# Performance work log

Hardware: AMD Instinct MI355X
Metric: run time of the kernel (lower is better)

## Reference

```python
import jax, jax.numpy as jnp
import numpy as np

GAMMA = 1.0  # weight on CRL loss
BETA = 1.0   # weight on MDCA calibration loss
B, C = 4096, 32000
DATASET_SIZE = 50000


def setup_inputs() -> dict:
    key = jax.random.key(0)
    k1, k2, k3, k4 = jax.random.split(key, 4)
    logits = jax.random.normal(k1, (B, C), dtype=jnp.float32)
    targets = jax.random.randint(k2, (B,), 0, C, dtype=jnp.int64)
    idx = jax.random.randint(k3, (B,), 0, DATASET_SIZE, dtype=jnp.int64)
    # normalized historical correctness per dataset sample (History table)
    correctness = jax.random.uniform(k4, (DATASET_SIZE,), dtype=jnp.float32)
    return {"logits": logits, "targets": targets, "idx": idx, "correctness": correctness}


def reference(logits, targets, idx, correctness):
    b, c = logits.shape
    logp = jax.nn.log_softmax(logits, axis=1)
    # CrossEntropyLoss (mean reduction)
    loss_cls = -jnp.mean(jnp.take_along_axis(logp, targets[:, None], axis=1))
    p = jnp.exp(logp)  # softmax probabilities, reused by MDCA and CRL

    # MDCA: mean_c | mean_b p[:, c] - freq(target == c) |, fused (no per-class loop)
    avg_conf = jnp.mean(p, axis=0)                                  # [C]
    avg_count = jnp.zeros((c,), logits.dtype).at[targets].add(1.0) / b  # [C]
    loss_cal = jnp.mean(jnp.abs(avg_conf - avg_count))

    # CRL (rank_target='softmax'): max-softmax confidence margin ranking
    conf = jnp.max(p, axis=1)          # [B]
    conf2 = jnp.roll(conf, -1)
    idx2 = jnp.roll(idx, -1)
    c1 = correctness[idx]
    c2 = correctness[idx2]
    rank_target = jnp.sign(c1 - c2)                     # {-1, 0, +1}
    rank_margin = jnp.abs(c1 - c2)
    tnz = jnp.where(rank_target == 0, jnp.ones_like(rank_target), rank_target)
    rank_input2 = conf2 + rank_margin / tnz
    # MarginRankingLoss(margin=0, mean): mean(max(0, -target*(x1 - x2)))
    loss_ref = jnp.mean(jnp.maximum(0.0, -rank_target * (conf - rank_input2)))

    return loss_cls + GAMMA * loss_ref + BETA * loss_cal
```

## Files before the change

### kernel.cpp

```cpp
#include <hip/hip_runtime.h>
#include <math.h>


#define NB  256
#define TPB 1024
#define NJ  8

__global__ __launch_bounds__(TPB) void fused_pass_kernel(
    const float* __restrict__ logits, const int* __restrict__ targets,
    float* __restrict__ partial,
    float* __restrict__ rowinv, float* __restrict__ celogp,
    float* __restrict__ counts, int B, int C)
{
    const int tid = threadIdx.x;
    const int n4  = C >> 2;
    const int rpb = B / NB;
    const int r0  = blockIdx.x * rpb;

    __shared__ float red[2][TPB / 64];
    __shared__ float sS[64];

    float4 acc[NJ];
    #pragma unroll
    for (int j = 0; j < NJ; ++j) acc[j] = make_float4(0.f, 0.f, 0.f, 0.f);

    const int wid = tid >> 6;

    float4 f[NJ], g[NJ];

    {
        const float4* row4 = (const float4*)(logits + (size_t)r0 * (size_t)C);
        #pragma unroll
        for (int j = 0; j < NJ; ++j) {
            const int k = tid + TPB * j;
            f[j] = (k < n4) ? row4[k] : make_float4(-1e30f, -1e30f, -1e30f, -1e30f);
        }
    }

    for (int r = 0; r < rpb; ++r) {
        if (r + 1 < rpb) {
            const float4* nrow =
                (const float4*)(logits + (size_t)(r0 + r + 1) * (size_t)C);
            #pragma unroll
            for (int j = 0; j < NJ; ++j) {
                const int k = tid + TPB * j;
                g[j] = (k < n4) ? nrow[k]
                                : make_float4(-1e30f, -1e30f, -1e30f, -1e30f);
            }
        }

        float ls = 0.f;
        #pragma unroll
        for (int j = 0; j < NJ; ++j) {
            f[j].x = __expf(f[j].x);
            f[j].y = __expf(f[j].y);
            f[j].z = __expf(f[j].z);
            f[j].w = __expf(f[j].w);
            ls += (f[j].x + f[j].y) + (f[j].z + f[j].w);
        }

        #pragma unroll
        for (int off = 32; off; off >>= 1) ls += __shfl_xor(ls, off, 64);
        const int par = r & 1;
        if ((tid & 63) == 0) red[par][wid] = ls;
        __syncthreads();
        float s = 0.f;
        #pragma unroll
        for (int w = 0; w < TPB / 64; ++w) s += red[par][w];
        if (tid == 0) sS[r] = s;
        const float inv = 1.0f / s;

        #pragma unroll
        for (int j = 0; j < NJ; ++j) {
            acc[j].x = fmaf(f[j].x, inv, acc[j].x);
            acc[j].y = fmaf(f[j].y, inv, acc[j].y);
            acc[j].z = fmaf(f[j].z, inv, acc[j].z);
            acc[j].w = fmaf(f[j].w, inv, acc[j].w);
        }

        if (r + 1 < rpb) {
            #pragma unroll
            for (int j = 0; j < NJ; ++j) f[j] = g[j];
        }
    }

    float4* po = (float4*)(partial + (size_t)blockIdx.x * (size_t)C);
    #pragma unroll
    for (int j = 0; j < NJ; ++j) {
        const int k = tid + TPB * j;
        if (k < n4) po[k] = acc[j];
    }

    __syncthreads();
    if (tid < rpb) {
        const int b = r0 + tid;
        const float s = sS[tid];
        rowinv[b] = 1.0f / s;
        const int t = targets[b];
        celogp[b] = logits[(size_t)b * (size_t)C + t] - logf(s);
        atomicAdd(&counts[t], 1.0f);
    }
}

__global__ __launch_bounds__(256) void reduce_cal_kernel(
    const float* __restrict__ partial, const float* __restrict__ counts,
    float* __restrict__ cal, int C)
{
    const int n4  = C >> 2;
    const int tid = threadIdx.x;
    const int c4  = blockIdx.x * 32 + (tid & 31);
    const int pg  = tid >> 5;

    const float4* p4   = (const float4*)partial;
    const float4* base = p4 + (size_t)(pg * (NB / 8)) * (size_t)n4 + c4;

    float4 s = make_float4(0.f, 0.f, 0.f, 0.f);
    #pragma unroll
    for (int p = 0; p < NB / 8; ++p) {
        const float4 v = base[(size_t)p * (size_t)n4];
        s.x += v.x; s.y += v.y; s.z += v.z; s.w += v.w;
    }

    __shared__ float4 lds[8][32];
    lds[pg][tid & 31] = s;
    __syncthreads();

    if (tid < 32) {
        float4 t = lds[0][tid];
        #pragma unroll
        for (int gi = 1; gi < 8; ++gi) {
            const float4 v = lds[gi][tid];
            t.x += v.x; t.y += v.y; t.z += v.z; t.w += v.w;
        }
        const float4 cnt = ((const float4*)counts)[c4];
        float d = fabsf(t.x - cnt.x) + fabsf(t.y - cnt.y)
                + fabsf(t.z - cnt.z) + fabsf(t.w - cnt.w);
        #pragma unroll
        for (int off = 16; off; off >>= 1) d += __shfl_xor(d, off, 64);
        if (tid == 0) atomicAdd(cal, d);
    }
}

__global__ __launch_bounds__(1024) void final_loss_kernel(
    const float* __restrict__ rowinv, const float* __restrict__ celogp,
    const int* __restrict__ idx, const float* __restrict__ correctness,
    const float* __restrict__ cal, float* __restrict__ out, int B, int C)
{
    const int tid = threadIdx.x;
    float sum_ce = 0.f, sum_crl = 0.f;

    for (int b = tid; b < B; b += 1024) {
        sum_ce += celogp[b];
        const int b2 = (b + 1 == B) ? 0 : b + 1;
        const float conf  = rowinv[b];
        const float conf2 = rowinv[b2];
        const float c1 = correctness[idx[b]];
        const float c2 = correctness[idx[b2]];
        const float rt  = (c1 > c2) ? 1.f : ((c1 < c2) ? -1.f : 0.f);
        const float rm  = fabsf(c1 - c2);
        const float tnz = (rt == 0.f) ? 1.f : rt;
        const float ri2 = conf2 + rm / tnz;
        sum_crl += fmaxf(0.f, -rt * (conf - ri2));
    }

    #pragma unroll
    for (int off = 32; off; off >>= 1) {
        sum_ce  += __shfl_xor(sum_ce,  off, 64);
        sum_crl += __shfl_xor(sum_crl, off, 64);
    }
    __shared__ float red[2][16];
    const int wid = tid >> 6;
    if ((tid & 63) == 0) { red[0][wid] = sum_ce; red[1][wid] = sum_crl; }
    __syncthreads();
    if (tid == 0) {
        float tce = 0.f, tcrl = 0.f;
        #pragma unroll
        for (int w = 0; w < 16; ++w) { tce += red[0][w]; tcrl += red[1][w]; }
        const float loss_cls = -tce / (float)B;
        const float loss_ref = tcrl / (float)B;
        const float loss_cal = cal[0] / ((float)B * (float)C);
        out[0] = loss_cls + loss_ref + loss_cal;
    }
}

extern "C" void kernel_launch(void* const* d_in, const int* in_sizes, int n_in,
                              void* d_out, int out_size, void* d_ws, size_t ws_size,
                              hipStream_t stream) {
    const float* logits      = (const float*)d_in[0];
    const int*   targets     = (const int*)d_in[1];
    const int*   idx         = (const int*)d_in[2];
    const float* correctness = (const float*)d_in[3];
    float* out = (float*)d_out;

    const int B = in_sizes[1];
    const int C = in_sizes[0] / B;

    char* ws = (char*)d_ws;
    float* partial = (float*)ws;   ws += (size_t)NB * (size_t)C * sizeof(float);
    float* rowinv  = (float*)ws;   ws += (size_t)B * sizeof(float);
    float* celogp  = (float*)ws;   ws += (size_t)B * sizeof(float);
    float* counts  = (float*)ws;   ws += (size_t)C * sizeof(float);
    float* cal     = (float*)ws;

    hipMemsetAsync(counts, 0, (size_t)C * sizeof(float), stream);
    hipMemsetAsync(cal, 0, sizeof(float), stream);

    fused_pass_kernel<<<NB, TPB, 0, stream>>>(logits, targets, partial,
                                              rowinv, celogp, counts, B, C);

    reduce_cal_kernel<<<(C >> 2) / 32, 256, 0, stream>>>(partial, counts, cal, C);

    final_loss_kernel<<<1, 1024, 0, stream>>>(rowinv, celogp, idx, correctness,
                                              cal, out, B, C);
}
```

Before: 791.2 us.

## Split fused pass into separate row-sum and column-sum kernels

Replaces the single fused kernel, which computed row sums and column accumulations with a block-wide barrier per row, with two kernels. The first kernel uses one block per row to compute the softmax denominator, CE term and target counts. The second re-reads the logits and accumulates the normalized exp per column using the precomputed inverse sums. This removes the per-row __syncthreads and register double-buffering and gives the row pass more parallelism, at the cost of reading the 524 MB logits matrix twice and computing exp twice.

```diff
diff --git a/kernel.cpp b/kernel.cpp
--- a/kernel.cpp
+++ b/kernel.cpp
@@ -6,81 +6,73 @@
 #define TPB 1024
 #define NJ  8
 
-__global__ __launch_bounds__(TPB) void fused_pass_kernel(
+__global__ __launch_bounds__(256) void rowsum_kernel(
     const float* __restrict__ logits, const int* __restrict__ targets,
-    float* __restrict__ partial,
     float* __restrict__ rowinv, float* __restrict__ celogp,
-    float* __restrict__ counts, int B, int C)
+    float* __restrict__ counts, int C)
+{
+    const int b   = blockIdx.x;
+    const int tid = threadIdx.x;
+    const int n4  = C >> 2;
+    const int nfull = n4 >> 8;
+    const int rem   = n4 - (nfull << 8);
+
+    const float4* row4 = (const float4*)(logits + (size_t)b * (size_t)C);
+
+    float ls = 0.f;
+    #pragma unroll 4
+    for (int i = 0; i < nfull; ++i) {
+        const float4 v = row4[tid + (i << 8)];
+        ls += (__expf(v.x) + __expf(v.y)) + (__expf(v.z) + __expf(v.w));
+    }
+    if (tid < rem) {
+        const float4 v = row4[(nfull << 8) + tid];
+        ls += (__expf(v.x) + __expf(v.y)) + (__expf(v.z) + __expf(v.w));
+    }
+
+    #pragma unroll
+    for (int off = 32; off; off >>= 1) ls += __shfl_xor(ls, off, 64);
+    __shared__ float red[4];
+    if ((tid & 63) == 0) red[tid >> 6] = ls;
+    __syncthreads();
+    if (tid == 0) {
+        const float s = red[0] + red[1] + red[2] + red[3];
+        rowinv[b] = 1.0f / s;
+        const int t = targets[b];
+        celogp[b] = logits[(size_t)b * (size_t)C + t] - logf(s);
+        atomicAdd(&counts[t], 1.0f);
+    }
+}
+
+__global__ __launch_bounds__(TPB) void colsum_kernel(
+    const float* __restrict__ logits, const float* __restrict__ rowinv,
+    float* __restrict__ partial, int B, int C)
 {
     const int tid = threadIdx.x;
     const int n4  = C >> 2;
     const int rpb = B / NB;
     const int r0  = blockIdx.x * rpb;
 
-    __shared__ float red[2][TPB / 64];
-    __shared__ float sS[64];
-
     float4 acc[NJ];
     #pragma unroll
     for (int j = 0; j < NJ; ++j) acc[j] = make_float4(0.f, 0.f, 0.f, 0.f);
 
-    const int wid = tid >> 6;
+    for (int r = 0; r < rpb; ++r) {
+        const float4* row4 = (const float4*)(logits + (size_t)(r0 + r) * (size_t)C);
+        const float inv = rowinv[r0 + r];
 
-    float4 f[NJ], g[NJ];
-
-    {
-        const float4* row4 = (const float4*)(logits + (size_t)r0 * (size_t)C);
+        float4 f[NJ];
         #pragma unroll
         for (int j = 0; j < NJ; ++j) {
             const int k = tid + TPB * j;
             f[j] = (k < n4) ? row4[k] : make_float4(-1e30f, -1e30f, -1e30f, -1e30f);
         }
-    }
-
-    for (int r = 0; r < rpb; ++r) {
-        if (r + 1 < rpb) {
-            const float4* nrow =
-                (const float4*)(logits + (size_t)(r0 + r + 1) * (size_t)C);
-            #pragma unroll
-            for (int j = 0; j < NJ; ++j) {
-                const int k = tid + TPB * j;
-                g[j] = (k < n4) ? nrow[k]
-                                : make_float4(-1e30f, -1e30f, -1e30f, -1e30f);
-            }
-        }
-
-        float ls = 0.f;
         #pragma unroll
         for (int j = 0; j < NJ; ++j) {
-            f[j].x = __expf(f[j].x);
-            f[j].y = __expf(f[j].y);
-            f[j].z = __expf(f[j].z);
-            f[j].w = __expf(f[j].w);
-            ls += (f[j].x + f[j].y) + (f[j].z + f[j].w);
-        }
-
-        #pragma unroll
-        for (int off = 32; off; off >>= 1) ls += __shfl_xor(ls, off, 64);
-        const int par = r & 1;
-        if ((tid & 63) == 0) red[par][wid] = ls;
-        __syncthreads();
-        float s = 0.f;
-        #pragma unroll
-        for (int w = 0; w < TPB / 64; ++w) s += red[par][w];
-        if (tid == 0) sS[r] = s;
-        const float inv = 1.0f / s;
-
-        #pragma unroll
-        for (int j = 0; j < NJ; ++j) {
-            acc[j].x = fmaf(f[j].x, inv, acc[j].x);
-            acc[j].y = fmaf(f[j].y, inv, acc[j].y);
-            acc[j].z = fmaf(f[j].z, inv, acc[j].z);
-            acc[j].w = fmaf(f[j].w, inv, acc[j].w);
-        }
-
-        if (r + 1 < rpb) {
-            #pragma unroll
-            for (int j = 0; j < NJ; ++j) f[j] = g[j];
+            acc[j].x = fmaf(__expf(f[j].x), inv, acc[j].x);
+            acc[j].y = fmaf(__expf(f[j].y), inv, acc[j].y);
+            acc[j].z = fmaf(__expf(f[j].z), inv, acc[j].z);
+            acc[j].w = fmaf(__expf(f[j].w), inv, acc[j].w);
         }
     }
 
@@ -89,16 +81,6 @@
     for (int j = 0; j < NJ; ++j) {
         const int k = tid + TPB * j;
         if (k < n4) po[k] = acc[j];
-    }
-
-    __syncthreads();
-    if (tid < rpb) {
-        const int b = r0 + tid;
-        const float s = sS[tid];
-        rowinv[b] = 1.0f / s;
-        const int t = targets[b];
-        celogp[b] = logits[(size_t)b * (size_t)C + t] - logf(s);
-        atomicAdd(&counts[t], 1.0f);
     }
 }
 
@@ -205,8 +187,10 @@
     hipMemsetAsync(counts, 0, (size_t)C * sizeof(float), stream);
     hipMemsetAsync(cal, 0, sizeof(float), stream);
 
-    fused_pass_kernel<<<NB, TPB, 0, stream>>>(logits, targets, partial,
-                                              rowinv, celogp, counts, B, C);
+    rowsum_kernel<<<B, 256, 0, stream>>>(logits, targets, rowinv, celogp,
+                                         counts, C);
+
+    colsum_kernel<<<NB, TPB, 0, stream>>>(logits, rowinv, partial, B, C);
 
     reduce_cal_kernel<<<(C >> 2) / 32, 256, 0, stream>>>(partial, counts, cal, C);
 
```

Measured after the change: 787.9 us. No clear change (-0.4%).

## Stash exp values as bf16 in LDS to drop prefetch register buffer

Applied to the files above, without the earlier changes.

The kernel now writes the exponentiated logits of each row to shared memory as packed bf16 instead of keeping them in registers. This frees the registers that held the next row, so the next-row load goes straight into the same register array. The aim is lower register pressure for 1024-thread blocks while keeping the load overlapped with the reduction. In exchange it adds LDS traffic and rounds probabilities to bf16, which reduces MDCA accuracy. The sS array also shrinks to 16 entries, which is only correct if rows per block is at most 16.

```diff
diff --git a/kernel.cpp b/kernel.cpp
--- a/kernel.cpp
+++ b/kernel.cpp
@@ -5,6 +5,14 @@
 #define NB  256
 #define TPB 1024
 #define NJ  8
+
+__device__ __forceinline__ unsigned int pack_bf16_rne(float a, float b) {
+    unsigned int ua = __float_as_uint(a);
+    unsigned int ub = __float_as_uint(b);
+    ua += 0x7FFFu + ((ua >> 16) & 1u);
+    ub += 0x7FFFu + ((ub >> 16) & 1u);
+    return (ua >> 16) | (ub & 0xFFFF0000u);
+}
 
 __global__ __launch_bounds__(TPB) void fused_pass_kernel(
     const float* __restrict__ logits, const int* __restrict__ targets,
@@ -17,8 +25,9 @@
     const int rpb = B / NB;
     const int r0  = blockIdx.x * rpb;
 
+    __shared__ unsigned int pbu[16000];
     __shared__ float red[2][TPB / 64];
-    __shared__ float sS[64];
+    __shared__ float sS[16];
 
     float4 acc[NJ];
     #pragma unroll
@@ -26,37 +35,40 @@
 
     const int wid = tid >> 6;
 
-    float4 f[NJ], g[NJ];
-
+    float4 f[NJ];
     {
         const float4* row4 = (const float4*)(logits + (size_t)r0 * (size_t)C);
         #pragma unroll
         for (int j = 0; j < NJ; ++j) {
             const int k = tid + TPB * j;
-            f[j] = (k < n4) ? row4[k] : make_float4(-1e30f, -1e30f, -1e30f, -1e30f);
+            if (k < n4) f[j] = row4[k];
         }
     }
 
     for (int r = 0; r < rpb; ++r) {
+        float ls = 0.f;
+        #pragma unroll
+        for (int j = 0; j < NJ; ++j) {
+            const int k = tid + TPB * j;
+            if (k < n4) {
+                const float ex = __expf(f[j].x), ey = __expf(f[j].y);
+                const float ez = __expf(f[j].z), ew = __expf(f[j].w);
+                ls += (ex + ey) + (ez + ew);
+                uint2 w;
+                w.x = pack_bf16_rne(ex, ey);
+                w.y = pack_bf16_rne(ez, ew);
+                *(uint2*)&pbu[2 * k] = w;
+            }
+        }
+
         if (r + 1 < rpb) {
-            const float4* nrow =
+            const float4* nr =
                 (const float4*)(logits + (size_t)(r0 + r + 1) * (size_t)C);
             #pragma unroll
             for (int j = 0; j < NJ; ++j) {
                 const int k = tid + TPB * j;
-                g[j] = (k < n4) ? nrow[k]
-                                : make_float4(-1e30f, -1e30f, -1e30f, -1e30f);
+                if (k < n4) f[j] = nr[k];
             }
-        }
-
-        float ls = 0.f;
-        #pragma unroll
-        for (int j = 0; j < NJ; ++j) {
-            f[j].x = __expf(f[j].x);
-            f[j].y = __expf(f[j].y);
-            f[j].z = __expf(f[j].z);
-            f[j].w = __expf(f[j].w);
-            ls += (f[j].x + f[j].y) + (f[j].z + f[j].w);
         }
 
         #pragma unroll
@@ -72,15 +84,18 @@
 
         #pragma unroll
         for (int j = 0; j < NJ; ++j) {
-            acc[j].x = fmaf(f[j].x, inv, acc[j].x);
-            acc[j].y = fmaf(f[j].y, inv, acc[j].y);
-            acc[j].z = fmaf(f[j].z, inv, acc[j].z);
-            acc[j].w = fmaf(f[j].w, inv, acc[j].w);
-        }
-
-        if (r + 1 < rpb) {
-            #pragma unroll
-            for (int j = 0; j < NJ; ++j) f[j] = g[j];
+            const int k = tid + TPB * j;
+            if (k < n4) {
+                const uint2 w = *(const uint2*)&pbu[2 * k];
+                const float px = __uint_as_float(w.x << 16);
+                const float py = __uint_as_float(w.x & 0xFFFF0000u);
+                const float pz = __uint_as_float(w.y << 16);
+                const float pw = __uint_as_float(w.y & 0xFFFF0000u);
+                acc[j].x = fmaf(px, inv, acc[j].x);
+                acc[j].y = fmaf(py, inv, acc[j].y);
+                acc[j].z = fmaf(pz, inv, acc[j].z);
+                acc[j].w = fmaf(pw, inv, acc[j].w);
+            }
         }
     }
 
```

After: 695.9 us. 12.0% less time.
